# Optimization experiments

Hardware: AMD Instinct MI355X
Metric: run time of the kernel (lower is better)

Reference implementation:

```python
import jax, jax.numpy as jnp
import numpy as np

N, L = 4, 512
DN = 128   # node_feat_dim
DP = 64    # pair_feat_dim
H = 8      # num_heads
HD = 32    # hidden_dim per head
EPS = 1e-5


def _layer_norm(x, g, b):
    m = jnp.mean(x, axis=-1, keepdims=True)
    v = jnp.var(x, axis=-1, keepdims=True)
    return (x - m) / jnp.sqrt(v + EPS) * g + b


def setup_inputs() -> dict:
    key = jax.random.key(0)
    ks = jax.random.split(key, 12)
    w = lambda k, shape: (jax.random.normal(k, shape, jnp.float32)
                          / np.float32(np.sqrt(shape[0])))
    return {
        "x": jax.random.normal(ks[0], (N, L, DN), jnp.float32),
        "z": jax.random.normal(ks[1], (N, L, L, DP), jnp.float32),
        "Wq": w(ks[2], (DN, H * HD)),
        "Wk": w(ks[3], (DN, H * HD)),
        "Wv": w(ks[4], (DN, H * HD)),
        "Wp": w(ks[5], (DP, H)),
        "Wt1": w(ks[6], (H * HD + H * DP, DN)),
        "bt1": jnp.zeros((DN,), jnp.float32),
        "g1": jnp.ones((DN,), jnp.float32),
        "b1": jnp.zeros((DN,), jnp.float32),
        "W2a": w(ks[7], (DN, DN)),
        "b2a": jnp.zeros((DN,), jnp.float32),
        "W2b": w(ks[8], (DN, DN)),
        "b2b": jnp.zeros((DN,), jnp.float32),
        "g2": jnp.ones((DN,), jnp.float32),
        "b2": jnp.zeros((DN,), jnp.float32),
    }


def reference(x, z, Wq, Wk, Wv, Wp, Wt1, bt1, g1, b1,
              W2a, b2a, W2b, b2b, g2, b2):
    # projections -> (N, L, H, HD)
    q = (x @ Wq).reshape(N, L, H, HD)
    k = (x @ Wk).reshape(N, L, H, HD)
    v = (x @ Wv).reshape(N, L, H, HD)
    # pairwise node logits: (N, Li, Lj, H)
    logits_node = jnp.einsum('nihd,njhd->nijh', q, k) / np.float32(np.sqrt(HD))
    logits_pair = z @ Wp                                    # (N, Li, Lj, H)
    logits = (logits_node + logits_pair) * np.float32(np.sqrt(0.5))
    alpha = jax.nn.softmax(logits, axis=2)                  # softmax over j
    # aggregation
    feat_node = jnp.einsum('nijh,njhd->nihd', alpha, v).reshape(N, L, H * HD)
    feat_pair = jnp.einsum('nijh,nijp->nihp', alpha, z).reshape(N, L, H * DP)
    agg = jnp.concatenate([feat_node, feat_pair], axis=-1)  # (N, L, H*HD + H*DP)
    feats = _layer_norm(x + agg @ Wt1 + bt1, g1, b1)
    out = jax.nn.relu(feats @ W2a + b2a) @ W2b + b2b
    return _layer_norm(feats + out, g2, b2)
```

## Files before the change

### kernel.cpp

```cpp
#include <hip/hip_runtime.h>
#include <math.h>

#define NB 4
#define L 512
#define DN 128
#define DP 64
#define H 8
#define HD 32
#define NH (H*HD)
#define AGG (NH + H*DP)
#define JC 64
#define NCH (L/JC)

__device__ float g_q[NB*L*NH];
__device__ float g_k[NB*L*NH];
__device__ float g_v[NB*L*NH];
__device__ float g_agg[NB*L*AGG];
__device__ float g_nl[(size_t)NB*H*L*L];

__global__ __launch_bounds__(256) void k_qkv(const float* __restrict__ x,
    const float* __restrict__ Wq, const float* __restrict__ Wk,
    const float* __restrict__ Wv)
{
    __shared__ float xs[4*DN];
    int t = threadIdx.x;
    int rowbase = blockIdx.x * 4;
    #pragma unroll
    for (int it = 0; it < 2; ++it) {
        int flat = it*256 + t;
        xs[flat] = x[(size_t)rowbase*DN + flat];
    }
    __syncthreads();
    float aq[4], ak[4], av[4];
    #pragma unroll
    for (int r = 0; r < 4; ++r) { aq[r]=0.f; ak[r]=0.f; av[r]=0.f; }
    for (int d = 0; d < DN; ++d) {
        float wq = Wq[d*NH + t];
        float wk = Wk[d*NH + t];
        float wv = Wv[d*NH + t];
        #pragma unroll
        for (int r = 0; r < 4; ++r) {
            float xv = xs[r*DN + d];
            aq[r] = fmaf(xv, wq, aq[r]);
            ak[r] = fmaf(xv, wk, ak[r]);
            av[r] = fmaf(xv, wv, av[r]);
        }
    }
    #pragma unroll
    for (int r = 0; r < 4; ++r) {
        g_q[(size_t)(rowbase+r)*NH + t] = aq[r] * 0.125f;
        g_k[(size_t)(rowbase+r)*NH + t] = ak[r];
        g_v[(size_t)(rowbase+r)*NH + t] = av[r];
    }
}

__global__ __launch_bounds__(256) void k_qk()
{
    __shared__ float qs[16*33];
    int t = threadIdx.x;
    int bid = blockIdx.x;
    int n = bid >> 8;
    int h = (bid >> 5) & 7;
    int i0 = (bid & 31) << 4;
    if (t < 128) {
        int row = t >> 3, c4 = (t & 7) << 2;
        const float4 qv = *(const float4*)(g_q + (size_t)(n*L + i0 + row)*NH + h*HD + c4);
        float* d = &qs[row*33 + c4];
        d[0]=qv.x; d[1]=qv.y; d[2]=qv.z; d[3]=qv.w;
    }
    __syncthreads();
    for (int jc = 0; jc < L; jc += 256) {
        int j = jc + t;
        float4 kr[8];
        const float4* kb = (const float4*)(g_k + (size_t)(n*L + j)*NH + h*HD);
        #pragma unroll
        for (int c4 = 0; c4 < 8; ++c4) kr[c4] = kb[c4];
        float* outb = g_nl + (size_t)((n*H + h)*L + i0)*L + j;
        #pragma unroll
        for (int i = 0; i < 16; ++i) {
            float acc = 0.f;
            #pragma unroll
            for (int c4 = 0; c4 < 8; ++c4) {
                const float* qp = &qs[i*33 + c4*4];
                acc = fmaf(qp[0], kr[c4].x, acc);
                acc = fmaf(qp[1], kr[c4].y, acc);
                acc = fmaf(qp[2], kr[c4].z, acc);
                acc = fmaf(qp[3], kr[c4].w, acc);
            }
            outb[(size_t)i*L] = acc;
        }
    }
}

#define ATTN_STEP(c, cur, NC0, NC4, NN0, NN4)                                  \
  {                                                                            \
    __syncthreads();                                                           \
    if ((c)+1 < NCH) {                                                         \
      _Pragma("unroll")                                                        \
      for (int it2 = 0; it2 < 4; ++it2) {                                      \
        int f4 = it2*256 + t, jj = f4 >> 4, p4 = (f4 & 15) << 2;               \
        float* d = &zc[(cur)^1][jj*65 + p4];                                   \
        d[0]=zR[it2].x; d[1]=zR[it2].y; d[2]=zR[it2].z; d[3]=zR[it2].w;        \
      }                                                                        \
    }                                                                          \
    if ((c)+2 < NCH) {                                                         \
      const float4* s2 = (const float4*)(zrow + (size_t)((c)+2)*JC*DP);        \
      zR[0]=s2[t]; zR[1]=s2[256+t]; zR[2]=s2[512+t]; zR[3]=s2[768+t];          \
    }                                                                          \
    if ((c)+1 < NCH) {                                                         \
      int jg2 = ((c)+1)*JC + lane;                                             \
      NN0 = nl0[jg2]; NN4 = nl4[jg2];                                          \
    }                                                                          \
    float va = NC0, vb = NC4;                                                  \
    {                                                                          \
      const float* zr = &zc[cur][lane*65];                                     \
      _Pragma("unroll 16")                                                     \
      for (int pp = 0; pp < DP; ++pp) {                                        \
        float zv = zr[pp];                                                     \
        va = fmaf(zv, wp[pp*H + wv],     va);                                  \
        vb = fmaf(zv, wp[pp*H + wv + 4], vb);                                  \
      }                                                                        \
    }                                                                          \
    float ma = va, mb = vb;                                                    \
    _Pragma("unroll")                                                          \
    for (int o = 32; o > 0; o >>= 1) {                                         \
      ma = fmaxf(ma, __shfl_xor(ma, o));                                       \
      mb = fmaxf(mb, __shfl_xor(mb, o));                                       \
    }                                                                          \
    float mna = fmaxf(m0, ma), mnb = fmaxf(m1, mb);                            \
    float ra = __expf(m0 - mna), rb = __expf(m1 - mnb);                        \
    float ea = __expf(va - mna), eb = __expf(vb - mnb);                        \
    lcw[wv][0][lane] = ea; lcw[wv][1][lane] = eb;                              \
    float sa = ea, sb = eb;                                                    \
    _Pragma("unroll")                                                          \
    for (int o = 32; o > 0; o >>= 1) {                                         \
      sa += __shfl_xor(sa, o); sb += __shfl_xor(sb, o);                        \
    }                                                                          \
    s0 = s0*ra + sa; s1 = s1*rb + sb; m0 = mna; m1 = mnb;                      \
    float rsel = (lane < 32) ? ra : rb;                                        \
    accN *= rsel; accP0 *= ra; accP1 *= rb;                                    \
    const float* vbase = g_v + (size_t)(n*L + (c)*JC)*NH + hoff;               \
    const float* zcc = zc[cur];                                                \
    _Pragma("unroll 8")                                                        \
    for (int j = 0; j < JC; ++j) {                                             \
      float la = lcw[wv][0][j];                                                \
      float lb = lcw[wv][1][j];                                                \
      float vv = vbase[(size_t)j*NH];                                          \
      float zv = zcc[j*65 + lane];                                             \
      float lsel = (lane < 32) ? la : lb;                                      \
      accN  = fmaf(lsel, vv, accN);                                            \
      accP0 = fmaf(la, zv, accP0);                                             \
      accP1 = fmaf(lb, zv, accP1);                                             \
    }                                                                          \
  }

__global__ __launch_bounds__(256) void k_attn(const float* __restrict__ z,
    const float* __restrict__ Wp)
{
    __shared__ float zc[2][JC*65];
    __shared__ float lcw[4][2][JC];
    __shared__ float wp[DP*H];

    int t = threadIdx.x;
    int lane = t & 63;
    int wv = t >> 6;
    int row = blockIdx.x;
    int n = row >> 9;
    int i = row & 511;
    const float* zrow = z + (size_t)row * (L*DP);

    wp[t]       = Wp[t]       * 0.70710678118654752f;
    wp[t + 256] = Wp[t + 256] * 0.70710678118654752f;

    const float* nl0 = g_nl + (size_t)((n*H + wv    )*L + i)*L;
    const float* nl4 = g_nl + (size_t)((n*H + wv + 4)*L + i)*L;

    int hoff = wv*32 + lane + ((lane < 32) ? 0 : 96);

    float accN = 0.f, accP0 = 0.f, accP1 = 0.f;
    float m0 = -1e30f, s0 = 0.f, m1 = -1e30f, s1 = 0.f;

    float4 zR[4];
    float nlc0, nlc4, nln0, nln4;

    {
        float4 zP[4];
        const float4* sp0 = (const float4*)zrow;
        #pragma unroll
        for (int it = 0; it < 4; ++it) zP[it] = sp0[it*256 + t];
        nlc0 = nl0[lane]; nlc4 = nl4[lane];
        #pragma unroll
        for (int it = 0; it < 4; ++it) {
            int f4 = it*256 + t, jj = f4 >> 4, p4 = (f4 & 15) << 2;
            float* d = &zc[0][jj*65 + p4];
            d[0]=zP[it].x; d[1]=zP[it].y; d[2]=zP[it].z; d[3]=zP[it].w;
        }
        const float4* sp1 = (const float4*)(zrow + (size_t)JC*DP);
        #pragma unroll
        for (int it = 0; it < 4; ++it) zR[it] = sp1[it*256 + t];
    }
    ATTN_STEP(0,0,nlc0,nlc4,nln0,nln4)
    ATTN_STEP(1,1,nln0,nln4,nlc0,nlc4)
    ATTN_STEP(2,0,nlc0,nlc4,nln0,nln4)
    ATTN_STEP(3,1,nln0,nln4,nlc0,nlc4)
    ATTN_STEP(4,0,nlc0,nlc4,nln0,nln4)
    ATTN_STEP(5,1,nln0,nln4,nlc0,nlc4)
    ATTN_STEP(6,0,nlc0,nlc4,nln0,nln4)
    ATTN_STEP(7,1,nln0,nln4,nlc0,nlc4)

    float* arow = g_agg + (size_t)row * AGG;
    float sn = (lane < 32) ? s0 : s1;
    arow[hoff]                  = accN  * (1.f / sn);
    arow[NH + wv*DP + lane]     = accP0 * (1.f / s0);
    arow[NH + (wv+4)*DP + lane] = accP1 * (1.f / s1);
}

__global__ __launch_bounds__(256) void k_mlp(const float* __restrict__ x,
    const float* __restrict__ Wt1, const float* __restrict__ bt1,
    const float* __restrict__ g1, const float* __restrict__ b1,
    const float* __restrict__ W2a, const float* __restrict__ b2a,
    const float* __restrict__ W2b, const float* __restrict__ b2b,
    const float* __restrict__ g2, const float* __restrict__ b2,
    float* __restrict__ out)
{
    __shared__ float aggL[4*AGG];
    __shared__ float featsL[4*132];
    __shared__ float h1L[4*132];
    int t = threadIdx.x;
    int tc = t & 127;
    int tr = t >> 7;
    int lane = t & 63, wv = t >> 6;
    int rowbase = blockIdx.x * 4;

    #pragma unroll
    for (int it = 0; it < 12; ++it) {
        int flat = it*256 + t;
        aggL[flat] = g_agg[(size_t)rowbase*AGG + flat];
    }
    __syncthreads();
    float acc[2] = {0.f,0.f};
    for (int kk = 0; kk < AGG; ++kk) {
        float w = Wt1[kk*DN + tc];
        #pragma unroll
        for (int r = 0; r < 2; ++r)
            acc[r] = fmaf(aggL[(tr*2+r)*AGG + kk], w, acc[r]);
    }
    float bt = bt1[tc];
    #pragma unroll
    for (int r = 0; r < 2; ++r) {
        int row = tr*2 + r;
        featsL[row*132 + tc] = acc[r] + bt + x[(size_t)(rowbase+row)*DN + tc];
    }
    __syncthreads();
    {
        int row = wv;
        float v0 = featsL[row*132 + lane];
        float v1 = featsL[row*132 + 64 + lane];
        float s = v0 + v1, s2 = v0*v0 + v1*v1;
        #pragma unroll
        for (int o = 32; o > 0; o >>= 1) {
            s  += __shfl_xor(s,  o);
            s2 += __shfl_xor(s2, o);
        }
        float mean = s * (1.f/128.f);
        float var  = s2 * (1.f/128.f) - mean*mean;
        float rstd = rsqrtf(var + 1e-5f);
        featsL[row*132 + lane]      = (v0 - mean)*rstd*g1[lane]      + b1[lane];
        featsL[row*132 + 64 + lane] = (v1 - mean)*rstd*g1[64+lane]   + b1[64+lane];
    }
    __syncthreads();
    float acc2[2] = {0.f,0.f};
    for (int kk = 0; kk < DN; ++kk) {
        float w = W2a[kk*DN + tc];
        #pragma unroll
        for (int r = 0; r < 2; ++r)
            acc2[r] = fmaf(featsL[(tr*2+r)*132 + kk], w, acc2[r]);
    }
    float ba = b2a[tc];
    #pragma unroll
    for (int r = 0; r < 2; ++r)
        h1L[(tr*2+r)*132 + tc] = fmaxf(acc2[r] + ba, 0.f);
    __syncthreads();
    float acc3[2] = {0.f,0.f};
    for (int kk = 0; kk < DN; ++kk) {
        float w = W2b[kk*DN + tc];
        #pragma unroll
        for (int r = 0; r < 2; ++r)
            acc3[r] = fmaf(h1L[(tr*2+r)*132 + kk], w, acc3[r]);
    }
    float bb = b2b[tc];
    #pragma unroll
    for (int r = 0; r < 2; ++r) {
        int row = tr*2 + r;
        featsL[row*132 + tc] = featsL[row*132 + tc] + acc3[r] + bb;
    }
    __syncthreads();
    {
        int row = wv;
        float v0 = featsL[row*132 + lane];
        float v1 = featsL[row*132 + 64 + lane];
        float s = v0 + v1, s2 = v0*v0 + v1*v1;
        #pragma unroll
        for (int o = 32; o > 0; o >>= 1) {
            s  += __shfl_xor(s,  o);
            s2 += __shfl_xor(s2, o);
        }
        float mean = s * (1.f/128.f);
        float var  = s2 * (1.f/128.f) - mean*mean;
        float rstd = rsqrtf(var + 1e-5f);
        out[(size_t)(rowbase+row)*DN + lane]      = (v0 - mean)*rstd*g2[lane]    + b2[lane];
        out[(size_t)(rowbase+row)*DN + 64 + lane] = (v1 - mean)*rstd*g2[64+lane] + b2[64+lane];
    }
}

extern "C" void kernel_launch(void* const* d_in, const int* in_sizes, int n_in,
                              void* d_out, int out_size, void* d_ws, size_t ws_size,
                              hipStream_t stream) {
    const float* x   = (const float*)d_in[0];
    const float* z   = (const float*)d_in[1];
    const float* Wq  = (const float*)d_in[2];
    const float* Wk  = (const float*)d_in[3];
    const float* Wv  = (const float*)d_in[4];
    const float* Wp  = (const float*)d_in[5];
    const float* Wt1 = (const float*)d_in[6];
    const float* bt1 = (const float*)d_in[7];
    const float* g1  = (const float*)d_in[8];
    const float* b1  = (const float*)d_in[9];
    const float* W2a = (const float*)d_in[10];
    const float* b2a = (const float*)d_in[11];
    const float* W2b = (const float*)d_in[12];
    const float* b2b = (const float*)d_in[13];
    const float* g2  = (const float*)d_in[14];
    const float* b2  = (const float*)d_in[15];
    float* out = (float*)d_out;

    k_qkv<<<NB*L/4, 256, 0, stream>>>(x, Wq, Wk, Wv);
    k_qk<<<NB*H*(L/16), 256, 0, stream>>>();
    k_attn<<<NB*L, 256, 0, stream>>>(z, Wp);
    k_mlp<<<NB*L/4, 256, 0, stream>>>(x, Wt1, bt1, g1, b1,
                                      W2a, b2a, W2b, b2b, g2, b2, out);
}
```

Baseline: 217.2 us.

## Transpose V and vectorize attention inner loops with split accumulators

V is now written transposed (head-dim major, sequence contiguous) so the attention kernel can load four consecutive j values per float4 instead of strided scalar loads. Wp is stored transposed in shared memory so the pair-logit dot product reads z and weights as float4 with two accumulator chains, and the softmax weights are interleaved so one float4 covers two j positions for both heads. The aggregation loop is rewritten with doubled accumulators to cut FMA dependency chains. The float4 reads of z rows at a 65-float stride are misaligned and may fault or be split into scalar loads, and the transposed V store in the QKV kernel becomes a strided scatter.

```diff
diff --git a/kernel.cpp b/kernel.cpp
--- a/kernel.cpp
+++ b/kernel.cpp
@@ -14,7 +14,7 @@
 
 __device__ float g_q[NB*L*NH];
 __device__ float g_k[NB*L*NH];
-__device__ float g_v[NB*L*NH];
+__device__ float g_vT[(size_t)NB*NH*L];
 __device__ float g_agg[NB*L*AGG];
 __device__ float g_nl[(size_t)NB*H*L*L];
 
@@ -50,8 +50,11 @@
     for (int r = 0; r < 4; ++r) {
         g_q[(size_t)(rowbase+r)*NH + t] = aq[r] * 0.125f;
         g_k[(size_t)(rowbase+r)*NH + t] = ak[r];
-        g_v[(size_t)(rowbase+r)*NH + t] = av[r];
-    }
+    }
+    int n2 = rowbase >> 9;
+    int i0 = rowbase & 511;
+    float4 v4 = make_float4(av[0], av[1], av[2], av[3]);
+    *(float4*)(g_vT + ((size_t)n2*NH + t)*L + i0) = v4;
 }
 
 __global__ __launch_bounds__(256) void k_qk()
@@ -111,16 +114,23 @@
       int jg2 = ((c)+1)*JC + lane;                                             \
       NN0 = nl0[jg2]; NN4 = nl4[jg2];                                          \
     }                                                                          \
-    float va = NC0, vb = NC4;                                                  \
+    float va = NC0, vb = NC4, va1 = 0.f, vb1 = 0.f;                            \
     {                                                                          \
-      const float* zr = &zc[cur][lane*65];                                     \
-      _Pragma("unroll 16")                                                     \
-      for (int pp = 0; pp < DP; ++pp) {                                        \
-        float zv = zr[pp];                                                     \
-        va = fmaf(zv, wp[pp*H + wv],     va);                                  \
-        vb = fmaf(zv, wp[pp*H + wv + 4], vb);                                  \
+      const float4* zr4 = (const float4*)&zc[cur][lane*65];                    \
+      _Pragma("unroll")                                                        \
+      for (int kk = 0; kk < 16; kk += 2) {                                     \
+        float4 z0 = zr4[kk], z1 = zr4[kk+1];                                   \
+        float4 wA0 = *(const float4*)&wpT[wv*64 + kk*4];                       \
+        float4 wB0 = *(const float4*)&wpT[(wv+4)*64 + kk*4];                   \
+        float4 wA1 = *(const float4*)&wpT[wv*64 + kk*4 + 4];                   \
+        float4 wB1 = *(const float4*)&wpT[(wv+4)*64 + kk*4 + 4];               \
+        va  = fmaf(z0.x,wA0.x,fmaf(z0.y,wA0.y,fmaf(z0.z,wA0.z,fmaf(z0.w,wA0.w,va))));   \
+        vb  = fmaf(z0.x,wB0.x,fmaf(z0.y,wB0.y,fmaf(z0.z,wB0.z,fmaf(z0.w,wB0.w,vb))));   \
+        va1 = fmaf(z1.x,wA1.x,fmaf(z1.y,wA1.y,fmaf(z1.z,wA1.z,fmaf(z1.w,wA1.w,va1)))); \
+        vb1 = fmaf(z1.x,wB1.x,fmaf(z1.y,wB1.y,fmaf(z1.z,wB1.z,fmaf(z1.w,wB1.w,vb1)))); \
       }                                                                        \
     }                                                                          \
+    va += va1; vb += vb1;                                                      \
     float ma = va, mb = vb;                                                    \
     _Pragma("unroll")                                                          \
     for (int o = 32; o > 0; o >>= 1) {                                         \
@@ -130,27 +140,35 @@
     float mna = fmaxf(m0, ma), mnb = fmaxf(m1, mb);                            \
     float ra = __expf(m0 - mna), rb = __expf(m1 - mnb);                        \
     float ea = __expf(va - mna), eb = __expf(vb - mnb);                        \
-    lcw[wv][0][lane] = ea; lcw[wv][1][lane] = eb;                              \
+    *(float2*)&lcw[wv][lane*2] = make_float2(ea, eb);                          \
     float sa = ea, sb = eb;                                                    \
     _Pragma("unroll")                                                          \
     for (int o = 32; o > 0; o >>= 1) {                                         \
       sa += __shfl_xor(sa, o); sb += __shfl_xor(sb, o);                        \
     }                                                                          \
     s0 = s0*ra + sa; s1 = s1*rb + sb; m0 = mna; m1 = mnb;                      \
-    float rsel = (lane < 32) ? ra : rb;                                        \
-    accN *= rsel; accP0 *= ra; accP1 *= rb;                                    \
-    const float* vbase = g_v + (size_t)(n*L + (c)*JC)*NH + hoff;               \
+    float rsel = hiHalf ? rb : ra;                                             \
+    accNa *= rsel; accNb *= rsel;                                              \
+    accP0a *= ra; accP0b *= ra; accP1a *= rb; accP1b *= rb;                    \
     const float* zcc = zc[cur];                                                \
-    _Pragma("unroll 8")                                                        \
-    for (int j = 0; j < JC; ++j) {                                             \
-      float la = lcw[wv][0][j];                                                \
-      float lb = lcw[wv][1][j];                                                \
-      float vv = vbase[(size_t)j*NH];                                          \
-      float zv = zcc[j*65 + lane];                                             \
-      float lsel = (lane < 32) ? la : lb;                                      \
-      accN  = fmaf(lsel, vv, accN);                                            \
-      accP0 = fmaf(la, zv, accP0);                                             \
-      accP1 = fmaf(lb, zv, accP1);                                             \
+    const float* vTb = vTrow + (c)*JC;                                         \
+    _Pragma("unroll")                                                          \
+    for (int jg = 0; jg < 16; ++jg) {                                          \
+      float4 lc0 = *(const float4*)&lcw[wv][jg*8];        \
+      float4 lc1 = *(const float4*)&lcw[wv][jg*8+4];      \
+      float4 vv  = *(const float4*)&vTb[jg*4];                                 \
+      const float* zp = &zcc[(4*jg)*65 + lane];                                \
+      float zv0 = zp[0], zv1 = zp[65], zv2 = zp[130], zv3 = zp[195];           \
+      float l0 = hiHalf ? lc0.y : lc0.x;                                       \
+      float l1 = hiHalf ? lc0.w : lc0.z;                                       \
+      float l2 = hiHalf ? lc1.y : lc1.x;                                       \
+      float l3 = hiHalf ? lc1.w : lc1.z;                                       \
+      accNa = fmaf(l0, vv.x, accNa); accNb = fmaf(l1, vv.y, accNb);            \
+      accNa = fmaf(l2, vv.z, accNa); accNb = fmaf(l3, vv.w, accNb);            \
+      accP0a = fmaf(lc0.x, zv0, accP0a); accP0b = fmaf(lc0.z, zv1, accP0b);    \
+      accP0a = fmaf(lc1.x, zv2, accP0a); accP0b = fmaf(lc1.z, zv3, accP0b);    \
+      accP1a = fmaf(lc0.y, zv0, accP1a); accP1b = fmaf(lc0.w, zv1, accP1b);    \
+      accP1a = fmaf(lc1.y, zv2, accP1a); accP1b = fmaf(lc1.w, zv3, accP1b);    \
     }                                                                          \
   }
 
@@ -158,8 +176,8 @@
     const float* __restrict__ Wp)
 {
     __shared__ float zc[2][JC*65];
-    __shared__ float lcw[4][2][JC];
-    __shared__ float wp[DP*H];
+    __shared__ float lcw[4][JC*2];
+    __shared__ float wpT[8*64];
 
     int t = threadIdx.x;
     int lane = t & 63;
@@ -169,15 +187,18 @@
     int i = row & 511;
     const float* zrow = z + (size_t)row * (L*DP);
 
-    wp[t]       = Wp[t]       * 0.70710678118654752f;
-    wp[t + 256] = Wp[t + 256] * 0.70710678118654752f;
+    wpT[t]       = Wp[(t & 63)*8 + (t >> 6)]        * 0.70710678118654752f;
+    wpT[t + 256] = Wp[(t & 63)*8 + ((t + 256) >> 6)] * 0.70710678118654752f;
 
     const float* nl0 = g_nl + (size_t)((n*H + wv    )*L + i)*L;
     const float* nl4 = g_nl + (size_t)((n*H + wv + 4)*L + i)*L;
 
-    int hoff = wv*32 + lane + ((lane < 32) ? 0 : 96);
-
-    float accN = 0.f, accP0 = 0.f, accP1 = 0.f;
+    bool hiHalf = (lane >= 32);
+    int hoff = wv*32 + lane + (hiHalf ? 96 : 0);
+    const float* vTrow = g_vT + ((size_t)n*NH + hoff)*L;
+
+    float accNa = 0.f, accNb = 0.f;
+    float accP0a = 0.f, accP0b = 0.f, accP1a = 0.f, accP1b = 0.f;
     float m0 = -1e30f, s0 = 0.f, m1 = -1e30f, s1 = 0.f;
 
     float4 zR[4];
@@ -208,8 +229,11 @@
     ATTN_STEP(6,0,nlc0,nlc4,nln0,nln4)
     ATTN_STEP(7,1,nln0,nln4,nlc0,nlc4)
 
+    float accN  = accNa + accNb;
+    float accP0 = accP0a + accP0b;
+    float accP1 = accP1a + accP1b;
     float* arow = g_agg + (size_t)row * AGG;
-    float sn = (lane < 32) ? s0 : s1;
+    float sn = hiHalf ? s1 : s0;
     arow[hoff]                  = accN  * (1.f / sn);
     arow[NH + wv*DP + lane]     = accP0 * (1.f / s0);
     arow[NH + (wv+4)*DP + lane] = accP1 * (1.f / s1);
```

New measurement: 437.7 us. 2.01x slower.
